# Performance work log

Measured on AMD Instinct MI355X. Metric: run time of the kernel, lower is better.

Reference implementation:

```python
import jax, jax.numpy as jnp
import numpy as np

N, E, F, H = 50000, 800000, 256, 64


def setup_inputs() -> dict:
    key = jax.random.key(0)
    ks = jax.random.split(key, 6)
    x = jax.random.normal(ks[0], (N, F), jnp.float32)
    edge_index = jax.random.randint(ks[1], (2, E), 0, N)
    init = lambda k, shp, fan: jax.random.normal(k, shp, jnp.float32) / np.float32(np.sqrt(fan))
    W1l = init(ks[2], (F, H), F)
    b1l = jnp.zeros((H,), jnp.float32)
    W1r = init(ks[3], (F, H), F)
    W2l = init(ks[4], (H, H), H)
    b2l = jnp.zeros((H,), jnp.float32)
    W2r = init(ks[5], (H, H), H)
    return dict(x=x, edge_index=edge_index, W1l=W1l, b1l=b1l, W1r=W1r,
                W2l=W2l, b2l=b2l, W2r=W2r)


def _sage(x, src, dst, Wl, bl, Wr, n):
    # SAGEConv: out = mean_{j->i}(lin_l(x)_j) + lin_r(x)_i
    m = x @ Wl + bl                                   # [N, H]
    agg = jax.ops.segment_sum(m[src], dst, num_segments=n)
    deg = jax.ops.segment_sum(jnp.ones((src.shape[0],), x.dtype), dst, num_segments=n)
    agg = agg / jnp.maximum(deg, 1.0)[:, None]        # mean aggregation
    return agg + x @ Wr


def reference(x, edge_index, W1l, b1l, W1r, W2l, b2l, W2r):
    src, dst = edge_index[0], edge_index[1]
    n = x.shape[0]
    # 2-layer SAGE encoder (dropout=0, no residual for 2 layers)
    h = jax.nn.relu(_sage(x, src, dst, W1l, b1l, W1r, n))
    z = _sage(h, src, dst, W2l, b2l, W2r, n)
    # UnitNorm: replace all-zero rows with randn, then row-wise L2 normalize
    valid = jnp.sum(z != 0, axis=1, keepdims=True) > 0
    r = jax.random.normal(jax.random.key(42), z.shape, z.dtype)
    z = jnp.where(valid, z, r)
    z = z / jnp.sqrt(jnp.sum(z * z, axis=1, keepdims=True))
    # dot-product decode on observed edges + positive-edge BCE loss
    scores = jnp.sum(z[src] * z[dst], axis=-1)        # [E]
    loss = -jnp.mean(jax.nn.log_sigmoid(scores))
    return z, loss
```

## Files before the change

kernel.cpp:

```cpp
#include <hip/hip_runtime.h>

#define N_NODES 50000
#define N_EDGES 800000
#define F_IN    256
#define H_DIM   64
#define NB_SCAN ((N_NODES + 255) / 256)
#define TILE_A  4096
#define EPT     (TILE_A / 256)
#define MAXB    5632
#define GT1     ((N_NODES + 63) / 64)
#define SUBN    64
#define DEC_GRID ((N_NODES + SUBN - 1) / SUBN)

typedef __attribute__((ext_vector_type(8))) short short8;
typedef __attribute__((ext_vector_type(4))) float floatx4;

__device__ __forceinline__ unsigned short f2bf(float f) {
  unsigned int u;
  __builtin_memcpy(&u, &f, 4);
  u += 0x7fffu + ((u >> 16) & 1u);
  return (unsigned short)(u >> 16);
}
__device__ __forceinline__ float bf2f(unsigned short s) {
  unsigned int v = ((unsigned int)s) << 16; float f; __builtin_memcpy(&f, &v, 4); return f;
}
__device__ __forceinline__ float bflo(unsigned int u) {
  unsigned int v = u << 16; float f; __builtin_memcpy(&f, &v, 4); return f;
}
__device__ __forceinline__ float bfhi(unsigned int u) {
  unsigned int v = u & 0xffff0000u; float f; __builtin_memcpy(&f, &v, 4); return f;
}

template<int K>
__device__ __forceinline__ void pack_body(int t, const float* __restrict__ Wl,
                                          const float* __restrict__ Wr,
                                          unsigned short* __restrict__ Wb)
{
  int lane = t & 63;
  int f    = t >> 6;
  int m    = f & 1;
  int c    = (f >> 1) & 3;
  int ks   = f >> 3;
  const float* W = m ? Wr : Wl;
  int quad = lane >> 4, l15 = lane & 15;
  int col = c * 16 + l15;
  unsigned short u[8];
#pragma unroll
  for (int j = 0; j < 8; ++j) {
    int k = ks * 32 + quad * 8 + j;
    u[j] = f2bf(W[k * H_DIM + col]);
  }
  uint4 v;
  __builtin_memcpy(&v, u, 16);
  ((uint4*)Wb)[t] = v;
}

__global__ __launch_bounds__(256) void pack_all_k(
    const float* __restrict__ W1l, const float* __restrict__ W1r,
    const float* __restrict__ W2l, const float* __restrict__ W2r,
    unsigned short* __restrict__ Wb1, unsigned short* __restrict__ Wb2,
    float* __restrict__ loss_slot, int* __restrict__ bcur)
{
  if (blockIdx.x == 0) {
    if (threadIdx.x == 0) loss_slot[0] = 0.f;
    if (threadIdx.x < NB_SCAN) bcur[threadIdx.x] = 0;
  }
  int b = blockIdx.x;
  if (b < 16) {
    pack_body<F_IN>(b * 256 + threadIdx.x, W1l, W1r, Wb1);
  } else {
    pack_body<H_DIM>((b - 16) * 256 + threadIdx.x, W2l, W2r, Wb2);
  }
}

template<int K, bool XBF16>
__device__ __forceinline__ void gemm_body(
    int bx, unsigned short* xs,
    const void* __restrict__ X_,
    const unsigned short* __restrict__ Wb,
    const float* __restrict__ bl,
    unsigned short* __restrict__ outl, unsigned short* __restrict__ outr)
{
  constexpr int KP = K + 8;
  const int row0 = bx * 64;
  if (XBF16) {
    const uint4* X = (const uint4*)X_;
    const int CH = K / 8;
    for (int i = threadIdx.x; i < 64 * CH; i += 256) {
      int r = i / CH, c = i % CH;
      int row = row0 + r;
      uint4 v = (row < N_NODES) ? X[(size_t)row * CH + c] : make_uint4(0, 0, 0, 0);
      *(uint4*)&xs[r * KP + c * 8] = v;
    }
  } else {
    const float4* X = (const float4*)X_;
    const int CH = K / 4;
    for (int i = threadIdx.x; i < 64 * CH; i += 256) {
      int r = i / CH, c = i % CH;
      int row = row0 + r;
      float4 v = (row < N_NODES) ? X[(size_t)row * CH + c]
                                 : make_float4(0.f, 0.f, 0.f, 0.f);
      unsigned int lo = (unsigned int)f2bf(v.x) | ((unsigned int)f2bf(v.y) << 16);
      unsigned int hi = (unsigned int)f2bf(v.z) | ((unsigned int)f2bf(v.w) << 16);
      *(uint2*)&xs[r * KP + c * 4] = make_uint2(lo, hi);
    }
// ... 10 lines not shown
#pragma unroll
  for (int c = 0; c < 4; ++c) { accl[c] = (floatx4)0.f; accr[c] = (floatx4)0.f; }

  const uint4* wbase = (const uint4*)Wb;
#pragma unroll
  for (int ks = 0; ks < K / 32; ++ks) {
    short8 af = *(const short8*)&xs[rloc * KP + ks * 32 + quad * 8];
#pragma unroll
    for (int c = 0; c < 4; ++c) {
      uint4 rl = wbase[((ks * 4 + c) * 2 + 0) * 64 + lane];
      uint4 rr = wbase[((ks * 4 + c) * 2 + 1) * 64 + lane];
      short8 bfl, bfr;
      __builtin_memcpy(&bfl, &rl, 16);
      __builtin_memcpy(&bfr, &rr, 16);
      accl[c] = __builtin_amdgcn_mfma_f32_16x16x32_bf16(af, bfl, accl[c], 0, 0, 0);
      accr[c] = __builtin_amdgcn_mfma_f32_16x16x32_bf16(af, bfr, accr[c], 0, 0, 0);
    }
  }
#pragma unroll
  for (int c = 0; c < 4; ++c) {
    int col = c * 16 + l15;
    float bias = bl[col];
#pragma unroll
    for (int reg = 0; reg < 4; ++reg) {
      int row = row0 + w * 16 + quad * 4 + reg;
      if (row < N_NODES) {
        outl[(size_t)row * H_DIM + col] = f2bf(accl[c][reg] + bias);
        outr[(size_t)row * H_DIM + col] = f2bf(accr[c][reg]);
      }
    }
  }
}

__global__ __launch_bounds__(256) void binA_k(const int* __restrict__ ei,
                                              int* __restrict__ bcur,
                                              unsigned int* __restrict__ ebuf)
{
  __shared__ int lcnt[256];
  __shared__ int lofs[256];
  __shared__ int lstart[256];
  __shared__ int gstart[256];
  __shared__ int lcur[256];
  __shared__ unsigned int ldata[TILE_A];
  const int t = threadIdx.x;
  const int e0 = blockIdx.x * TILE_A;
  lcnt[t] = 0;
  __syncthreads();
  int ss[EPT], ds[EPT];
#pragma unroll
  for (int j = 0; j < EPT; ++j) {
    int e = e0 + t + j * 256;
    if (e < N_EDGES) {
      ss[j] = ei[e];
      ds[j] = ei[N_EDGES + e];
      atomicAdd(&lcnt[ds[j] >> 8], 1);
    } else {
      ds[j] = -1;
    }
  }
  __syncthreads();
  int v = lcnt[t];
  lofs[t] = v;
  __syncthreads();
  for (int off = 1; off < 256; off <<= 1) {
    int u = (t >= off) ? lofs[t - off] : 0;
    __syncthreads();
    lofs[t] += u;
    __syncthreads();
  }
  lstart[t] = lofs[t] - v;
  lcur[t]   = lofs[t] - v;
  if (t < NB_SCAN && v > 0) gstart[t] = atomicAdd(&bcur[t], v);
  __syncthreads();
#pragma unroll
  for (int j = 0; j < EPT; ++j) {
    if (ds[j] >= 0) {
      int p = atomicAdd(&lcur[ds[j] >> 8], 1);
      ldata[p] = ((unsigned int)ss[j] << 8) | (unsigned int)(ds[j] & 255);
// ... 38 lines not shown
  __syncthreads();
  const int start = sh_se[0], len = sh_se[1];
  const unsigned int* eb = ebuf + (size_t)b * MAXB;
  ncnt[t] = 0;
  __syncthreads();
  for (int i = t; i < len; i += 256) atomicAdd(&ncnt[eb[i] & 255], 1);
  __syncthreads();
  int v = ncnt[t];
  nscan[t] = v;
  __syncthreads();
  for (int off = 1; off < 256; off <<= 1) {
    int u = (t >= off) ? nscan[t - off] : 0;
    __syncthreads();
    nscan[t] += u;
    __syncthreads();
  }
  ncur[t] = nscan[t] - v;
  __syncthreads();
  for (int i = t; i < len; i += 256) {
    unsigned int e = eb[i];
    int p = atomicAdd(&ncur[e & 255], 1);
    sdata[p] = e >> 8;
  }
  __syncthreads();
  for (int i = t; i < len; i += 256) esrc[start + i] = (int)sdata[i];
  int node = b * 256 + t;
  int s0 = start + nscan[t] - v;
  if (node < N_NODES) {
    rowptr[node] = s0;
    if (node == N_NODES - 1) rowptr[N_NODES] = s0 + v;
  }
}

__global__ __launch_bounds__(256, 4) void binB_gemm1_k(
    const float* __restrict__ x, const unsigned short* __restrict__ Wb1,
    const float* __restrict__ b1l,
    unsigned short* __restrict__ m1, unsigned short* __restrict__ xr,
    const unsigned int* __restrict__ ebuf, const int* __restrict__ bcur,
    int* __restrict__ esrc, int* __restrict__ rowptr)
{
  __shared__ __align__(16) unsigned char smem[64 * (F_IN + 8) * 2];
  if (blockIdx.x < GT1) {
    gemm_body<F_IN, false>(blockIdx.x, (unsigned short*)smem, x, Wb1, b1l, m1, xr);
  } else {
    binB_body(blockIdx.x - GT1, smem, ebuf, bcur, esrc, rowptr);
  }
}

__global__ __launch_bounds__(256, 4) void gemm2_k(
    const void* __restrict__ X_, const unsigned short* __restrict__ Wb,
    const float* __restrict__ bl,
    unsigned short* __restrict__ outl, unsigned short* __restrict__ outr)
{
  __shared__ __align__(16) unsigned short xs[64 * (H_DIM + 8)];
  gemm_body<H_DIM, true>(blockIdx.x, xs, X_, Wb, bl, outl, outr);
}

__device__ __forceinline__ void agg_quad(const int* __restrict__ esrc,
                                         const unsigned short* __restrict__ m,
                                         int b, int e, int g, int l15,
                                         float* __restrict__ a)
{
  float a0 = 0.f, a1 = 0.f, a2 = 0.f, a3 = 0.f;
  float b0 = 0.f, b1 = 0.f, b2 = 0.f, b3 = 0.f;
  int i = b + g;
  for (; i + 4 < e; i += 8) {
    int s0 = esrc[i], s1 = esrc[i + 4];
    uint2 v0 = *(const uint2*)(m + (size_t)s0 * H_DIM + l15 * 4);
    uint2 v1 = *(const uint2*)(m + (size_t)s1 * H_DIM + l15 * 4);
    a0 += bflo(v0.x); a1 += bfhi(v0.x); a2 += bflo(v0.y); a3 += bfhi(v0.y);
    b0 += bflo(v1.x); b1 += bfhi(v1.x); b2 += bflo(v1.y); b3 += bfhi(v1.y);
  }
  if (i < e) {
    int s0 = esrc[i];
    uint2 v0 = *(const uint2*)(m + (size_t)s0 * H_DIM + l15 * 4);
    a0 += bflo(v0.x); a1 += bfhi(v0.x); a2 += bflo(v0.y); a3 += bfhi(v0.y);
  }
  a[0] = a0 + b0; a[1] = a1 + b1; a[2] = a2 + b2; a[3] = a3 + b3;
#pragma unroll
  for (int j = 0; j < 4; ++j) {
    a[j] += __shfl_xor(a[j], 16, 64);
    a[j] += __shfl_xor(a[j], 32, 64);
  }
}

__global__ __launch_bounds__(256) void agg1_k(
    const int* __restrict__ rowptr, const int* __restrict__ esrc,
    const unsigned short* __restrict__ m, const unsigned short* __restrict__ xr,
    unsigned short* __restrict__ h)
{
  int gid = blockIdx.x * 256 + threadIdx.x;
  int row = gid >> 6;
  if (row >= N_NODES) return;
  int lane = threadIdx.x & 63, g = lane >> 4, l15 = lane & 15;
  int b = rowptr[row], e = rowptr[row + 1];
  float a[4];
  agg_quad(esrc, m, b, e, g, l15, a);
  if (g == 0) {
    float dv = fmaxf((float)(e - b), 1.f);
    float inv = 1.f / dv;
    uint2 rx = *(const uint2*)(xr + (size_t)row * H_DIM + l15 * 4);
    float h0 = fmaxf(a[0] * inv + bflo(rx.x), 0.f);
    float h1 = fmaxf(a[1] * inv + bfhi(rx.x), 0.f);
    float h2 = fmaxf(a[2] * inv + bflo(rx.y), 0.f);
    float h3 = fmaxf(a[3] * inv + bfhi(rx.y), 0.f);
    uint2 o;
    o.x = (unsigned int)f2bf(h0) | ((unsigned int)f2bf(h1) << 16);
    o.y = (unsigned int)f2bf(h2) | ((unsigned int)f2bf(h3) << 16);
    *(uint2*)(h + (size_t)row * H_DIM + l15 * 4) = o;
  }
}

__global__ __launch_bounds__(256) void agg2_k(
    const int* __restrict__ rowptr, const int* __restrict__ esrc,
    const unsigned short* __restrict__ m, const unsigned short* __restrict__ hr,
    float* __restrict__ zout, unsigned short* __restrict__ zb)
{
  int gid = blockIdx.x * 256 + threadIdx.x;
  int row = gid >> 6;
  if (row >= N_NODES) return;
  int lane = threadIdx.x & 63, g = lane >> 4, l15 = lane & 15;
  int b = rowptr[row], e = rowptr[row + 1];
  float a[4];
  agg_quad(esrc, m, b, e, g, l15, a);
  float dv = fmaxf((float)(e - b), 1.f);
  float inv = 1.f / dv;
  uint2 rx = *(const uint2*)(hr + (size_t)row * H_DIM + l15 * 4);
  float v0 = a[0] * inv + bflo(rx.x);
  float v1 = a[1] * inv + bfhi(rx.x);
  float v2 = a[2] * inv + bflo(rx.y);
  float v3 = a[3] * inv + bfhi(rx.y);
  float ss = v0 * v0 + v1 * v1 + v2 * v2 + v3 * v3;
#pragma unroll
  for (int mm = 8; mm >= 1; mm >>= 1) ss += __shfl_xor(ss, mm, 64);
  float rs = rsqrtf(fmaxf(ss, 1e-30f));
  if (g == 0) {
    float z0 = v0 * rs, z1 = v1 * rs, z2 = v2 * rs, z3 = v3 * rs;
    *(float4*)(zout + (size_t)row * H_DIM + l15 * 4) = make_float4(z0, z1, z2, z3);
    uint2 o;
    o.x = (unsigned int)f2bf(z0) | ((unsigned int)f2bf(z1) << 16);
    o.y = (unsigned int)f2bf(z2) | ((unsigned int)f2bf(z3) << 16);
    *(uint2*)(zb + (size_t)row * H_DIM + l15 * 4) = o;
  }
}

__global__ __launch_bounds__(256) void decode_lds_k(
    const int* __restrict__ rowptr, const int* __restrict__ esrc,
    const unsigned short* __restrict__ zb, float* __restrict__ loss_slot)
{
  __shared__ __align__(16) uint4 zrows[SUBN * 8];
  __shared__ int sh_rp[SUBN + 1];
  const int t = threadIdx.x;
  const int node0 = blockIdx.x * SUBN;
  const int nr = min(SUBN, N_NODES - node0);
  for (int i = t; i < nr * 8; i += 256) {
    int r = i >> 3, c = i & 7;
    uint4 v = ((const uint4*)(zb + (size_t)(node0 + r) * H_DIM))[c];
    zrows[r * 8 + (c ^ (r & 7))] = v;
  }
  if (t <= nr) sh_rp[t] = rowptr[node0 + t];
  __syncthreads();
  const int estart = sh_rp[0], eend = sh_rp[nr];
  float part = 0.f;
  for (int e = estart + t; e < eend; e += 512) {
    int e2 = e + 256;
    bool has2 = (e2 < eend);
    int lo = 0, hi = nr;
    while (hi - lo > 1) {
      int mid = (lo + hi) >> 1;
      if (sh_rp[mid] <= e) lo = mid; else hi = mid;
    }
    const int r1 = lo;
    hi = nr;
    while (hi - lo > 1) {
      int mid = (lo + hi) >> 1;
      if (sh_rp[mid] <= e2) lo = mid; else hi = mid;
    }
    const int r2 = lo;
    const int s1 = esrc[e];
    const int s2 = has2 ? esrc[e2] : s1;
    const uint4* zs1 = (const uint4*)(zb + (size_t)s1 * H_DIM);
    const uint4* zs2 = (const uint4*)(zb + (size_t)s2 * H_DIM);
    float p1 = 0.f, p2 = 0.f;
#pragma unroll
    for (int c = 0; c < 8; ++c) {
      uint4 a1 = zs1[c], b1 = zrows[r1 * 8 + (c ^ (r1 & 7))];
      uint4 a2 = zs2[c], b2 = zrows[r2 * 8 + (c ^ (r2 & 7))];
      unsigned int au1[4] = {a1.x, a1.y, a1.z, a1.w};
      unsigned int bu1[4] = {b1.x, b1.y, b1.z, b1.w};
      unsigned int au2[4] = {a2.x, a2.y, a2.z, a2.w};
      unsigned int bu2[4] = {b2.x, b2.y, b2.z, b2.w};
#pragma unroll
      for (int j = 0; j < 4; ++j) {
        p1 = fmaf(bflo(au1[j]), bflo(bu1[j]), p1);
        p1 = fmaf(bfhi(au1[j]), bfhi(bu1[j]), p1);
        p2 = fmaf(bflo(au2[j]), bflo(bu2[j]), p2);
        p2 = fmaf(bfhi(au2[j]), bfhi(bu2[j]), p2);
      }
    }
    part += fmaxf(-p1, 0.f) + log1pf(expf(-fabsf(p1)));
    if (has2) part += fmaxf(-p2, 0.f) + log1pf(expf(-fabsf(p2)));
  }
#pragma unroll
  for (int m = 32; m >= 1; m >>= 1) part += __shfl_xor(part, m, 64);
  __shared__ float sbuf[4];
  int lane = t & 63, w = t >> 6;
  if (lane == 0) sbuf[w] = part;
  __syncthreads();
  if (t == 0)
    atomicAdd(loss_slot, (sbuf[0] + sbuf[1] + sbuf[2] + sbuf[3]) * (1.0f / N_EDGES));
}

extern "C" void kernel_launch(void* const* d_in, const int* in_sizes, int n_in,
                              void* d_out, int out_size, void* d_ws, size_t ws_size,
                              hipStream_t stream)
{
  (void)in_sizes; (void)n_in; (void)out_size; (void)ws_size;
  const float* x   = (const float*)d_in[0];
  const int*   ei  = (const int*)d_in[1];
  const float* W1l = (const float*)d_in[2];
  const float* b1l = (const float*)d_in[3];
  const float* W1r = (const float*)d_in[4];
  const float* W2l = (const float*)d_in[5];
  const float* b2l = (const float*)d_in[6];
  const float* W2r = (const float*)d_in[7];
  float* out = (float*)d_out;
  float* loss_slot = out + (size_t)N_NODES * H_DIM;

  const size_t NH = (size_t)N_NODES * H_DIM;
  unsigned short* uA = (unsigned short*)d_ws;
  unsigned short* uB = uA + NH;
  unsigned short* uC = uB + NH;
  unsigned short* Wb1 = uC + NH;
  unsigned short* Wb2 = Wb1 + (F_IN / 32) * 4 * 2 * 64 * 8;
  int* rowptr = (int*)(Wb2 + (H_DIM / 32) * 4 * 2 * 64 * 8);
  int* esrc   = rowptr + N_NODES + 1;
  int* bcur   = esrc + N_EDGES;
  unsigned int* ebuf = (unsigned int*)(bcur + NB_SCAN);

  dim3 blk(256);
  dim3 g_node((N_NODES * 64 + 255) / 256);
  dim3 g_binA((N_EDGES + TILE_A - 1) / TILE_A);
  dim3 g_fuse(GT1 + NB_SCAN);
  dim3 g_tile(GT1);
  dim3 g_dec(DEC_GRID);

  pack_all_k<<<dim3(20), blk, 0, stream>>>(W1l, W1r, W2l, W2r, Wb1, Wb2,
                                           loss_slot, bcur);
  binA_k<<<g_binA, blk, 0, stream>>>(ei, bcur, ebuf);
  binB_gemm1_k<<<g_fuse, blk, 0, stream>>>(x, Wb1, b1l, uA, uC,
                                           ebuf, bcur, esrc, rowptr);
  agg1_k<<<g_node, blk, 0, stream>>>(rowptr, esrc, uA, uC, uB);
  gemm2_k<<<g_tile, blk, 0, stream>>>(uB, Wb2, b2l, uA, uC);
  agg2_k<<<g_node, blk, 0, stream>>>(rowptr, esrc, uA, uC, out, uB);
  decode_lds_k<<<g_dec, blk, 0, stream>>>(rowptr, esrc, uB, loss_slot);
}
```

Before: 236.7 us.

## Fuse all stages into one cooperative persistent kernel with grid syncs

Replaces the seven separate kernel launches with a single cooperative persistent kernel that loops over work items for each stage and separates the stages with grid-wide barriers. It also halves the binA edge tile. The aim is to remove per-launch overhead and the gaps between dependent kernels. The trade-offs are lower occupancy, because the grid is capped by co-resident blocks and the kernel needs registers for every stage, plus grid-sync cost and load imbalance inside each phase. The old multi-kernel path is kept as a fallback.

Result: slower. 715.1 us (+202.1%).

```diff
diff --git a/kernel.cpp b/kernel.cpp
--- a/kernel.cpp
+++ b/kernel.cpp
@@ -1,16 +1,22 @@
 #include <hip/hip_runtime.h>
+#include <hip/hip_cooperative_groups.h>
+
+namespace cg = cooperative_groups;
 
 #define N_NODES 50000
 #define N_EDGES 800000
 #define F_IN    256
 #define H_DIM   64
 #define NB_SCAN ((N_NODES + 255) / 256)
-#define TILE_A  4096
+#define TILE_A  2048
 #define EPT     (TILE_A / 256)
+#define NT_A    ((N_EDGES + TILE_A - 1) / TILE_A)
 #define MAXB    5632
 #define GT1     ((N_NODES + 63) / 64)
 #define SUBN    64
 #define DEC_GRID ((N_NODES + SUBN - 1) / SUBN)
+#define AGG_VB  ((N_NODES + 3) / 4)
+#define SMEM_BYTES (64 * (F_IN + 8) * 2)
 
 typedef __attribute__((ext_vector_type(8))) short short8;
 typedef __attribute__((ext_vector_type(4))) float floatx4;
@@ -30,6 +36,7 @@
 __device__ __forceinline__ float bfhi(unsigned int u) {
   unsigned int v = u & 0xffff0000u; float f; __builtin_memcpy(&f, &v, 4); return f;
 }
+
 
 template<int K>
 __device__ __forceinline__ void pack_body(int t, const float* __restrict__ Wl,
@@ -53,24 +60,6 @@
   uint4 v;
   __builtin_memcpy(&v, u, 16);
   ((uint4*)Wb)[t] = v;
-}
-
-__global__ __launch_bounds__(256) void pack_all_k(
-    const float* __restrict__ W1l, const float* __restrict__ W1r,
-    const float* __restrict__ W2l, const float* __restrict__ W2r,
-    unsigned short* __restrict__ Wb1, unsigned short* __restrict__ Wb2,
-    float* __restrict__ loss_slot, int* __restrict__ bcur)
-{
-  if (blockIdx.x == 0) {
-    if (threadIdx.x == 0) loss_slot[0] = 0.f;
-    if (threadIdx.x < NB_SCAN) bcur[threadIdx.x] = 0;
-  }
-  int b = blockIdx.x;
-  if (b < 16) {
-    pack_body<F_IN>(b * 256 + threadIdx.x, W1l, W1r, Wb1);
-  } else {
-    pack_body<H_DIM>((b - 16) * 256 + threadIdx.x, W2l, W2r, Wb2);
-  }
 }
 
 template<int K, bool XBF16>
@@ -147,18 +136,19 @@
   }
 }
 
-__global__ __launch_bounds__(256) void binA_k(const int* __restrict__ ei,
-                                              int* __restrict__ bcur,
-                                              unsigned int* __restrict__ ebuf)
-{
-  __shared__ int lcnt[256];
-  __shared__ int lofs[256];
-  __shared__ int lstart[256];
-  __shared__ int gstart[256];
-  __shared__ int lcur[256];
-  __shared__ unsigned int ldata[TILE_A];
+__device__ __forceinline__ void binA_body(int blk, unsigned char* smem,
+                                          const int* __restrict__ ei,
+                                          int* __restrict__ bcur,
+                                          unsigned int* __restrict__ ebuf)
+{
+  int* lcnt   = (int*)smem;
+  int* lofs   = lcnt + 256;
+  int* lstart = lofs + 256;
+  int* gstart = lstart + 256;
+  int* lcur   = gstart + 256;
+  unsigned int* ldata = (unsigned int*)(lcur + 256);
   const int t = threadIdx.x;
-  const int e0 = blockIdx.x * TILE_A;
+  const int e0 = blk * TILE_A;
   lcnt[t] = 0;
   __syncthreads();
   int ss[EPT], ds[EPT];
@@ -263,30 +253,6 @@
   }
 }
 
-__global__ __launch_bounds__(256, 4) void binB_gemm1_k(
-    const float* __restrict__ x, const unsigned short* __restrict__ Wb1,
-    const float* __restrict__ b1l,
-    unsigned short* __restrict__ m1, unsigned short* __restrict__ xr,
-    const unsigned int* __restrict__ ebuf, const int* __restrict__ bcur,
-    int* __restrict__ esrc, int* __restrict__ rowptr)
-{
-  __shared__ __align__(16) unsigned char smem[64 * (F_IN + 8) * 2];
-  if (blockIdx.x < GT1) {
-    gemm_body<F_IN, false>(blockIdx.x, (unsigned short*)smem, x, Wb1, b1l, m1, xr);
-  } else {
-    binB_body(blockIdx.x - GT1, smem, ebuf, bcur, esrc, rowptr);
-  }
-}
-
-__global__ __launch_bounds__(256, 4) void gemm2_k(
-    const void* __restrict__ X_, const unsigned short* __restrict__ Wb,
-    const float* __restrict__ bl,
-    unsigned short* __restrict__ outl, unsigned short* __restrict__ outr)
-{
-  __shared__ __align__(16) unsigned short xs[64 * (H_DIM + 8)];
-  gemm_body<H_DIM, true>(blockIdx.x, xs, X_, Wb, bl, outl, outr);
-}
-
 __device__ __forceinline__ void agg_quad(const int* __restrict__ esrc,
                                          const unsigned short* __restrict__ m,
                                          int b, int e, int g, int l15,
@@ -315,21 +281,16 @@
   }
 }
 
-__global__ __launch_bounds__(256) void agg1_k(
+__device__ __forceinline__ void agg1_row(int row,
     const int* __restrict__ rowptr, const int* __restrict__ esrc,
     const unsigned short* __restrict__ m, const unsigned short* __restrict__ xr,
-    unsigned short* __restrict__ h)
-{
-  int gid = blockIdx.x * 256 + threadIdx.x;
-  int row = gid >> 6;
-  if (row >= N_NODES) return;
-  int lane = threadIdx.x & 63, g = lane >> 4, l15 = lane & 15;
+    unsigned short* __restrict__ h, int g, int l15)
+{
   int b = rowptr[row], e = rowptr[row + 1];
   float a[4];
   agg_quad(esrc, m, b, e, g, l15, a);
   if (g == 0) {
-    float dv = fmaxf((float)(e - b), 1.f);
-    float inv = 1.f / dv;
+    float inv = 1.f / fmaxf((float)(e - b), 1.f);
     uint2 rx = *(const uint2*)(xr + (size_t)row * H_DIM + l15 * 4);
     float h0 = fmaxf(a[0] * inv + bflo(rx.x), 0.f);
     float h1 = fmaxf(a[1] * inv + bfhi(rx.x), 0.f);
@@ -342,20 +303,15 @@
   }
 }
 
-__global__ __launch_bounds__(256) void agg2_k(
+__device__ __forceinline__ void agg2_row(int row,
     const int* __restrict__ rowptr, const int* __restrict__ esrc,
     const unsigned short* __restrict__ m, const unsigned short* __restrict__ hr,
-    float* __restrict__ zout, unsigned short* __restrict__ zb)
-{
-  int gid = blockIdx.x * 256 + threadIdx.x;
-  int row = gid >> 6;
-  if (row >= N_NODES) return;
-  int lane = threadIdx.x & 63, g = lane >> 4, l15 = lane & 15;
+    float* __restrict__ zout, unsigned short* __restrict__ zb, int g, int l15)
+{
   int b = rowptr[row], e = rowptr[row + 1];
   float a[4];
   agg_quad(esrc, m, b, e, g, l15, a);
-  float dv = fmaxf((float)(e - b), 1.f);
-  float inv = 1.f / dv;
+  float inv = 1.f / fmaxf((float)(e - b), 1.f);
   uint2 rx = *(const uint2*)(hr + (size_t)row * H_DIM + l15 * 4);
   float v0 = a[0] * inv + bflo(rx.x);
   float v1 = a[1] * inv + bfhi(rx.x);
@@ -375,14 +331,15 @@
   }
 }
 
-__global__ __launch_bounds__(256) void decode_lds_k(
+__device__ __forceinline__ void decode_body(int wb, unsigned char* smem,
     const int* __restrict__ rowptr, const int* __restrict__ esrc,
     const unsigned short* __restrict__ zb, float* __restrict__ loss_slot)
 {
-  __shared__ __align__(16) uint4 zrows[SUBN * 8];
-  __shared__ int sh_rp[SUBN + 1];
+  uint4* zrows = (uint4*)smem;
+  int*   sh_rp = (int*)(smem + 8192);
+  float* sbuf  = (float*)(smem + 8192 + 272);
   const int t = threadIdx.x;
-  const int node0 = blockIdx.x * SUBN;
+  const int node0 = wb * SUBN;
   const int nr = min(SUBN, N_NODES - node0);
   for (int i = t; i < nr * 8; i += 256) {
     int r = i >> 3, c = i & 7;
@@ -434,12 +391,151 @@
   }
 #pragma unroll
   for (int m = 32; m >= 1; m >>= 1) part += __shfl_xor(part, m, 64);
-  __shared__ float sbuf[4];
   int lane = t & 63, w = t >> 6;
   if (lane == 0) sbuf[w] = part;
   __syncthreads();
   if (t == 0)
     atomicAdd(loss_slot, (sbuf[0] + sbuf[1] + sbuf[2] + sbuf[3]) * (1.0f / N_EDGES));
+}
+
+__global__ __launch_bounds__(256, 4) void mega_k(
+    const float* __restrict__ x, const int* __restrict__ ei,
+    const float* __restrict__ W1l, const float* __restrict__ b1l,
+    const float* __restrict__ W1r, const float* __restrict__ W2l,
+    const float* __restrict__ b2l, const float* __restrict__ W2r,
+    float* __restrict__ out, float* __restrict__ loss_slot,
+    unsigned short* __restrict__ uA, unsigned short* __restrict__ uB,
+    unsigned short* __restrict__ uC, unsigned short* __restrict__ Wb1,
+    unsigned short* __restrict__ Wb2, int* __restrict__ rowptr,
+    int* __restrict__ esrc, int* __restrict__ bcur,
+    unsigned int* __restrict__ ebuf)
+{
+  __shared__ __align__(16) unsigned char smem[SMEM_BYTES];
+  cg::grid_group gg = cg::this_grid();
+  const int t = threadIdx.x;
+  const int lane = t & 63, qg = lane >> 4, l15 = lane & 15, wv = t >> 6;
+
+  if (blockIdx.x < 16) {
+    pack_body<F_IN>(blockIdx.x * 256 + t, W1l, W1r, Wb1);
+  } else if (blockIdx.x < 20) {
+    pack_body<H_DIM>((blockIdx.x - 16) * 256 + t, W2l, W2r, Wb2);
+  } else if (blockIdx.x == 20) {
+    if (t == 0) loss_slot[0] = 0.f;
+    if (t < NB_SCAN) bcur[t] = 0;
+  }
+  gg.sync();
+
+  for (int blk = blockIdx.x; blk < NT_A; blk += gridDim.x) {
+    binA_body(blk, smem, ei, bcur, ebuf);
+    __syncthreads();
+  }
+  gg.sync();
+
+  for (int w = blockIdx.x; w < GT1 + NB_SCAN; w += gridDim.x) {
+    if (w < GT1) gemm_body<F_IN, false>(w, (unsigned short*)smem, x, Wb1, b1l, uA, uC);
+    else         binB_body(w - GT1, smem, ebuf, bcur, esrc, rowptr);
+    __syncthreads();
+  }
+  gg.sync();
+
+  for (int vb = blockIdx.x; vb < AGG_VB; vb += gridDim.x) {
+    int row = vb * 4 + wv;
+    if (row < N_NODES) agg1_row(row, rowptr, esrc, uA, uC, uB, qg, l15);
+  }
+  gg.sync();
+
+  for (int bx = blockIdx.x; bx < GT1; bx += gridDim.x) {
+    gemm_body<H_DIM, true>(bx, (unsigned short*)smem, uB, Wb2, b2l, uA, uC);
+    __syncthreads();
+  }
+  gg.sync();
+
+  for (int vb = blockIdx.x; vb < AGG_VB; vb += gridDim.x) {
+    int row = vb * 4 + wv;
+    if (row < N_NODES) agg2_row(row, rowptr, esrc, uA, uC, out, uB, qg, l15);
+  }
+  gg.sync();
+
+  for (int w = blockIdx.x; w < DEC_GRID; w += gridDim.x) {
+    decode_body(w, smem, rowptr, esrc, uB, loss_slot);
+    __syncthreads();
+  }
+}
+
+__global__ __launch_bounds__(256) void pack_all_k(
+    const float* __restrict__ W1l, const float* __restrict__ W1r,
+    const float* __restrict__ W2l, const float* __restrict__ W2r,
+    unsigned short* __restrict__ Wb1, unsigned short* __restrict__ Wb2,
+    float* __restrict__ loss_slot, int* __restrict__ bcur)
+{
+  if (blockIdx.x == 0) {
+    if (threadIdx.x == 0) loss_slot[0] = 0.f;
+    if (threadIdx.x < NB_SCAN) bcur[threadIdx.x] = 0;
+  }
+  int b = blockIdx.x;
+  if (b < 16) pack_body<F_IN>(b * 256 + threadIdx.x, W1l, W1r, Wb1);
+  else        pack_body<H_DIM>((b - 16) * 256 + threadIdx.x, W2l, W2r, Wb2);
+}
+
+__global__ __launch_bounds__(256) void binA_k(const int* __restrict__ ei,
+                                              int* __restrict__ bcur,
+                                              unsigned int* __restrict__ ebuf)
+{
+  __shared__ __align__(16) unsigned char smem[5 * 1024 + TILE_A * 4];
+  binA_body(blockIdx.x, smem, ei, bcur, ebuf);
+}
+
+__global__ __launch_bounds__(256, 4) void binB_gemm1_k(
+    const float* __restrict__ x, const unsigned short* __restrict__ Wb1,
+    const float* __restrict__ b1l,
+    unsigned short* __restrict__ m1, unsigned short* __restrict__ xr,
+    const unsigned int* __restrict__ ebuf, const int* __restrict__ bcur,
+    int* __restrict__ esrc, int* __restrict__ rowptr)
+{
+  __shared__ __align__(16) unsigned char smem[SMEM_BYTES];
+  if (blockIdx.x < GT1) gemm_body<F_IN, false>(blockIdx.x, (unsigned short*)smem, x, Wb1, b1l, m1, xr);
+  else                  binB_body(blockIdx.x - GT1, smem, ebuf, bcur, esrc, rowptr);
+}
+
+__global__ __launch_bounds__(256, 4) void gemm2_k(
+    const void* __restrict__ X_, const unsigned short* __restrict__ Wb,
+    const float* __restrict__ bl,
+    unsigned short* __restrict__ outl, unsigned short* __restrict__ outr)
+{
+  __shared__ __align__(16) unsigned short xs[64 * (H_DIM + 8)];
+  gemm_body<H_DIM, true>(blockIdx.x, xs, X_, Wb, bl, outl, outr);
+}
+
+__global__ __launch_bounds__(256) void agg1_k(
+    const int* __restrict__ rowptr, const int* __restrict__ esrc,
+    const unsigned short* __restrict__ m, const unsigned short* __restrict__ xr,
+    unsigned short* __restrict__ h)
+{
+  int gid = blockIdx.x * 256 + threadIdx.x;
+  int row = gid >> 6;
+  if (row >= N_NODES) return;
+  int lane = threadIdx.x & 63;
+  agg1_row(row, rowptr, esrc, m, xr, h, lane >> 4, lane & 15);
+}
+
+__global__ __launch_bounds__(256) void agg2_k(
+    const int* __restrict__ rowptr, const int* __restrict__ esrc,
+    const unsigned short* __restrict__ m, const unsigned short* __restrict__ hr,
+    float* __restrict__ zout, unsigned short* __restrict__ zb)
+{
+  int gid = blockIdx.x * 256 + threadIdx.x;
+  int row = gid >> 6;
+  if (row >= N_NODES) return;
+  int lane = threadIdx.x & 63;
+  agg2_row(row, rowptr, esrc, m, hr, zout, zb, lane >> 4, lane & 15);
+}
+
+__global__ __launch_bounds__(256) void decode_lds_k(
+    const int* __restrict__ rowptr, const int* __restrict__ esrc,
+    const unsigned short* __restrict__ zb, float* __restrict__ loss_slot)
+{
+  __shared__ __align__(16) unsigned char smem[8480];
+  decode_body(blockIdx.x, smem, rowptr, esrc, zb, loss_slot);
 }
 
 extern "C" void kernel_launch(void* const* d_in, const int* in_sizes, int n_in,
@@ -469,20 +565,41 @@
   int* bcur   = esrc + N_EDGES;
   unsigned int* ebuf = (unsigned int*)(bcur + NB_SCAN);
 
-  dim3 blk(256);
-  dim3 g_node((N_NODES * 64 + 255) / 256);
-  dim3 g_binA((N_EDGES + TILE_A - 1) / TILE_A);
-  dim3 g_fuse(GT1 + NB_SCAN);
-  dim3 g_tile(GT1);
-  dim3 g_dec(DEC_GRID);
-
-  pack_all_k<<<dim3(20), blk, 0, stream>>>(W1l, W1r, W2l, W2r, Wb1, Wb2,
-                                           loss_slot, bcur);
-  binA_k<<<g_binA, blk, 0, stream>>>(ei, bcur, ebuf);
-  binB_gemm1_k<<<g_fuse, blk, 0, stream>>>(x, Wb1, b1l, uA, uC,
-                                           ebuf, bcur, esrc, rowptr);
-  agg1_k<<<g_node, blk, 0, stream>>>(rowptr, esrc, uA, uC, uB);
-  gemm2_k<<<g_tile, blk, 0, stream>>>(uB, Wb2, b2l, uA, uC);
-  agg2_k<<<g_node, blk, 0, stream>>>(rowptr, esrc, uA, uC, out, uB);
-  decode_lds_k<<<g_dec, blk, 0, stream>>>(rowptr, esrc, uB, loss_slot);
-}
+  static int g_grid = 0;
+  if (g_grid == 0) {
+    int nb = 0;
+    hipError_t e = hipOccupancyMaxActiveBlocksPerMultiprocessor(&nb, mega_k, 256, 0);
+    int dev = 0;
+    hipGetDevice(&dev);
+    hipDeviceProp_t prop;
+    hipGetDeviceProperties(&prop, dev);
+    long cap = (e == hipSuccess && nb > 0) ? (long)nb * prop.multiProcessorCount : 0;
+    g_grid = (cap <= 0) ? -1 : (int)(cap < 1024 ? cap : 1024);
+  }
+
+  bool coop_ok = false;
+  if (g_grid > 0) {
+    void* params[] = {
+      (void*)&x, (void*)&ei, (void*)&W1l, (void*)&b1l, (void*)&W1r,
+      (void*)&W2l, (void*)&b2l, (void*)&W2r, (void*)&out, (void*)&loss_slot,
+      (void*)&uA, (void*)&uB, (void*)&uC, (void*)&Wb1, (void*)&Wb2,
+      (void*)&rowptr, (void*)&esrc, (void*)&bcur, (void*)&ebuf};
+    hipError_t e = hipLaunchCooperativeKernel((const void*)mega_k, dim3(g_grid),
+                                              dim3(256), params, 0, stream);
+    coop_ok = (e == hipSuccess);
+    if (!coop_ok) g_grid = -1;
+  }
+
+  if (!coop_ok) {
+    dim3 blk(256);
+    pack_all_k<<<dim3(20), blk, 0, stream>>>(W1l, W1r, W2l, W2r, Wb1, Wb2,
+                                             loss_slot, bcur);
+    binA_k<<<dim3(NT_A), blk, 0, stream>>>(ei, bcur, ebuf);
+    binB_gemm1_k<<<dim3(GT1 + NB_SCAN), blk, 0, stream>>>(x, Wb1, b1l, uA, uC,
+                                                          ebuf, bcur, esrc, rowptr);
+    agg1_k<<<dim3((N_NODES * 64 + 255) / 256), blk, 0, stream>>>(rowptr, esrc, uA, uC, uB);
+    gemm2_k<<<dim3(GT1), blk, 0, stream>>>(uB, Wb2, b2l, uA, uC);
+    agg2_k<<<dim3((N_NODES * 64 + 255) / 256), blk, 0, stream>>>(rowptr, esrc, uA, uC, out, uB);
+    decode_lds_k<<<dim3(DEC_GRID), blk, 0, stream>>>(rowptr, esrc, uB, loss_slot);
+  }
+}
```

## Fuse layer-1 aggregation with layer-2 GEMM and unroll gather loop deeper

Applied to the files above, without the earlier changes.

Merges the first-layer mean aggregation and the second-layer dual linear projection into one kernel. Each 512-thread block aggregates 64 rows into shared memory as bf16 h, then four waves run MFMA against the packed W2 weights, so h is never written to or re-read from global memory and one launch goes away. New buffers uD/uE are used to avoid read/write aliasing with the layer-1 outputs. The gather loop in agg_quad now keeps four independent accumulator sets and issues four loads per iteration for more memory-level parallelism. The cost is fewer blocks (one per 64 rows) with half the waves idle during the GEMM phase, and more register pressure in the gather loop.

New measurement: 255.9 us. 1.08x slower.

```diff
diff --git a/kernel.cpp b/kernel.cpp
--- a/kernel.cpp
+++ b/kernel.cpp
@@ -66,11 +66,8 @@
     if (threadIdx.x < NB_SCAN) bcur[threadIdx.x] = 0;
   }
   int b = blockIdx.x;
-  if (b < 16) {
-    pack_body<F_IN>(b * 256 + threadIdx.x, W1l, W1r, Wb1);
-  } else {
-    pack_body<H_DIM>((b - 16) * 256 + threadIdx.x, W2l, W2r, Wb2);
-  }
+  if (b < 16) pack_body<F_IN>(b * 256 + threadIdx.x, W1l, W1r, Wb1);
+  else        pack_body<H_DIM>((b - 16) * 256 + threadIdx.x, W2l, W2r, Wb2);
 }
 
 template<int K, bool XBF16>
@@ -271,20 +268,8 @@
     int* __restrict__ esrc, int* __restrict__ rowptr)
 {
   __shared__ __align__(16) unsigned char smem[64 * (F_IN + 8) * 2];
-  if (blockIdx.x < GT1) {
-    gemm_body<F_IN, false>(blockIdx.x, (unsigned short*)smem, x, Wb1, b1l, m1, xr);
-  } else {
-    binB_body(blockIdx.x - GT1, smem, ebuf, bcur, esrc, rowptr);
-  }
-}
-
-__global__ __launch_bounds__(256, 4) void gemm2_k(
-    const void* __restrict__ X_, const unsigned short* __restrict__ Wb,
-    const float* __restrict__ bl,
-    unsigned short* __restrict__ outl, unsigned short* __restrict__ outr)
-{
-  __shared__ __align__(16) unsigned short xs[64 * (H_DIM + 8)];
-  gemm_body<H_DIM, true>(blockIdx.x, xs, X_, Wb, bl, outl, outr);
+  if (blockIdx.x < GT1) gemm_body<F_IN, false>(blockIdx.x, (unsigned short*)smem, x, Wb1, b1l, m1, xr);
+  else                  binB_body(blockIdx.x - GT1, smem, ebuf, bcur, esrc, rowptr);
 }
 
 __device__ __forceinline__ void agg_quad(const int* __restrict__ esrc,
@@ -292,22 +277,31 @@
                                          int b, int e, int g, int l15,
                                          float* __restrict__ a)
 {
-  float a0 = 0.f, a1 = 0.f, a2 = 0.f, a3 = 0.f;
-  float b0 = 0.f, b1 = 0.f, b2 = 0.f, b3 = 0.f;
+  float p0 = 0.f, p1 = 0.f, p2 = 0.f, p3 = 0.f;
+  float q0 = 0.f, q1 = 0.f, q2 = 0.f, q3 = 0.f;
+  float r0 = 0.f, r1 = 0.f, r2 = 0.f, r3 = 0.f;
+  float s0 = 0.f, s1 = 0.f, s2 = 0.f, s3 = 0.f;
   int i = b + g;
-  for (; i + 4 < e; i += 8) {
-    int s0 = esrc[i], s1 = esrc[i + 4];
-    uint2 v0 = *(const uint2*)(m + (size_t)s0 * H_DIM + l15 * 4);
-    uint2 v1 = *(const uint2*)(m + (size_t)s1 * H_DIM + l15 * 4);
-    a0 += bflo(v0.x); a1 += bfhi(v0.x); a2 += bflo(v0.y); a3 += bfhi(v0.y);
-    b0 += bflo(v1.x); b1 += bfhi(v1.x); b2 += bflo(v1.y); b3 += bfhi(v1.y);
-  }
-  if (i < e) {
-    int s0 = esrc[i];
-    uint2 v0 = *(const uint2*)(m + (size_t)s0 * H_DIM + l15 * 4);
-    a0 += bflo(v0.x); a1 += bfhi(v0.x); a2 += bflo(v0.y); a3 += bfhi(v0.y);
-  }
-  a[0] = a0 + b0; a[1] = a1 + b1; a[2] = a2 + b2; a[3] = a3 + b3;
+  for (; i + 12 < e; i += 16) {
+    int sa = esrc[i], sb = esrc[i + 4], sc = esrc[i + 8], sd = esrc[i + 12];
+    uint2 va = *(const uint2*)(m + (size_t)sa * H_DIM + l15 * 4);
+    uint2 vb = *(const uint2*)(m + (size_t)sb * H_DIM + l15 * 4);
+    uint2 vc = *(const uint2*)(m + (size_t)sc * H_DIM + l15 * 4);
+    uint2 vd = *(const uint2*)(m + (size_t)sd * H_DIM + l15 * 4);
+    p0 += bflo(va.x); p1 += bfhi(va.x); p2 += bflo(va.y); p3 += bfhi(va.y);
+    q0 += bflo(vb.x); q1 += bfhi(vb.x); q2 += bflo(vb.y); q3 += bfhi(vb.y);
+    r0 += bflo(vc.x); r1 += bfhi(vc.x); r2 += bflo(vc.y); r3 += bfhi(vc.y);
+    s0 += bflo(vd.x); s1 += bfhi(vd.x); s2 += bflo(vd.y); s3 += bfhi(vd.y);
+  }
+  for (; i < e; i += 4) {
+    int sa = esrc[i];
+    uint2 va = *(const uint2*)(m + (size_t)sa * H_DIM + l15 * 4);
+    p0 += bflo(va.x); p1 += bfhi(va.x); p2 += bflo(va.y); p3 += bfhi(va.y);
+  }
+  a[0] = (p0 + q0) + (r0 + s0);
+  a[1] = (p1 + q1) + (r1 + s1);
+  a[2] = (p2 + q2) + (r2 + s2);
+  a[3] = (p3 + q3) + (r3 + s3);
 #pragma unroll
   for (int j = 0; j < 4; ++j) {
     a[j] += __shfl_xor(a[j], 16, 64);
@@ -315,10 +309,86 @@
   }
 }
 
-__global__ __launch_bounds__(256) void agg1_k(
+__global__ __launch_bounds__(512) void agg1gemm2_k(
     const int* __restrict__ rowptr, const int* __restrict__ esrc,
-    const unsigned short* __restrict__ m, const unsigned short* __restrict__ xr,
-    unsigned short* __restrict__ h)
+    const unsigned short* __restrict__ m1, const unsigned short* __restrict__ xr,
+    const unsigned short* __restrict__ Wb, const float* __restrict__ bl,
+    unsigned short* __restrict__ outl, unsigned short* __restrict__ outr)
+{
+  constexpr int KP = H_DIM + 8;
+  __shared__ __align__(16) unsigned short xs[64 * KP];
+  const int t = threadIdx.x;
+  const int wv = t >> 6;
+  const int lane = t & 63;
+  const int g = lane >> 4, l15 = lane & 15;
+  const int row0 = blockIdx.x * 64;
+
+  for (int k = 0; k < 8; ++k) {
+    int r = wv * 8 + k;
+    int row = row0 + r;
+    if (row < N_NODES) {
+      int b = rowptr[row], e = rowptr[row + 1];
+      float a[4];
+      agg_quad(esrc, m1, b, e, g, l15, a);
+      if (g == 0) {
+        float inv = 1.f / fmaxf((float)(e - b), 1.f);
+        uint2 rx = *(const uint2*)(xr + (size_t)row * H_DIM + l15 * 4);
+        float h0 = fmaxf(a[0] * inv + bflo(rx.x), 0.f);
+        float h1 = fmaxf(a[1] * inv + bfhi(rx.x), 0.f);
+        float h2 = fmaxf(a[2] * inv + bflo(rx.y), 0.f);
+        float h3 = fmaxf(a[3] * inv + bfhi(rx.y), 0.f);
+        uint2 o;
+        o.x = (unsigned int)f2bf(h0) | ((unsigned int)f2bf(h1) << 16);
+        o.y = (unsigned int)f2bf(h2) | ((unsigned int)f2bf(h3) << 16);
+        *(uint2*)&xs[r * KP + l15 * 4] = o;
+      }
+    } else if (g == 0) {
+      *(uint2*)&xs[r * KP + l15 * 4] = make_uint2(0u, 0u);
+    }
+  }
+  __syncthreads();
+
+  if (wv < 4) {
+    const int quad = lane >> 4;
+    const int rloc = wv * 16 + l15;
+    floatx4 accl[4], accr[4];
+#pragma unroll
+    for (int c = 0; c < 4; ++c) { accl[c] = (floatx4)0.f; accr[c] = (floatx4)0.f; }
+    const uint4* wbase = (const uint4*)Wb;
+#pragma unroll
+    for (int ks = 0; ks < 2; ++ks) {
+      short8 af = *(const short8*)&xs[rloc * KP + ks * 32 + quad * 8];
+#pragma unroll
+      for (int c = 0; c < 4; ++c) {
+        uint4 rl = wbase[((ks * 4 + c) * 2 + 0) * 64 + lane];
+        uint4 rr = wbase[((ks * 4 + c) * 2 + 1) * 64 + lane];
+        short8 bfl, bfr;
+        __builtin_memcpy(&bfl, &rl, 16);
+        __builtin_memcpy(&bfr, &rr, 16);
+        accl[c] = __builtin_amdgcn_mfma_f32_16x16x32_bf16(af, bfl, accl[c], 0, 0, 0);
+        accr[c] = __builtin_amdgcn_mfma_f32_16x16x32_bf16(af, bfr, accr[c], 0, 0, 0);
+      }
+    }
+#pragma unroll
+    for (int c = 0; c < 4; ++c) {
+      int col = c * 16 + l15;
+      float bias = bl[col];
+#pragma unroll
+      for (int reg = 0; reg < 4; ++reg) {
+        int row = row0 + wv * 16 + quad * 4 + reg;
+        if (row < N_NODES) {
+          outl[(size_t)row * H_DIM + col] = f2bf(accl[c][reg] + bias);
+          outr[(size_t)row * H_DIM + col] = f2bf(accr[c][reg]);
+        }
+      }
+    }
+  }
+}
+
+__global__ __launch_bounds__(256) void agg2_k(
+    const int* __restrict__ rowptr, const int* __restrict__ esrc,
+    const unsigned short* __restrict__ m, const unsigned short* __restrict__ hr,
+    float* __restrict__ zout, unsigned short* __restrict__ zb)
 {
   int gid = blockIdx.x * 256 + threadIdx.x;
   int row = gid >> 6;
@@ -327,35 +397,7 @@
   int b = rowptr[row], e = rowptr[row + 1];
   float a[4];
   agg_quad(esrc, m, b, e, g, l15, a);
-  if (g == 0) {
-    float dv = fmaxf((float)(e - b), 1.f);
-    float inv = 1.f / dv;
-    uint2 rx = *(const uint2*)(xr + (size_t)row * H_DIM + l15 * 4);
-    float h0 = fmaxf(a[0] * inv + bflo(rx.x), 0.f);
-    float h1 = fmaxf(a[1] * inv + bfhi(rx.x), 0.f);
-    float h2 = fmaxf(a[2] * inv + bflo(rx.y), 0.f);
-    float h3 = fmaxf(a[3] * inv + bfhi(rx.y), 0.f);
-    uint2 o;
-    o.x = (unsigned int)f2bf(h0) | ((unsigned int)f2bf(h1) << 16);
-    o.y = (unsigned int)f2bf(h2) | ((unsigned int)f2bf(h3) << 16);
-    *(uint2*)(h + (size_t)row * H_DIM + l15 * 4) = o;
-  }
-}
-
-__global__ __launch_bounds__(256) void agg2_k(
-    const int* __restrict__ rowptr, const int* __restrict__ esrc,
-    const unsigned short* __restrict__ m, const unsigned short* __restrict__ hr,
-    float* __restrict__ zout, unsigned short* __restrict__ zb)
-{
-  int gid = blockIdx.x * 256 + threadIdx.x;
-  int row = gid >> 6;
-  if (row >= N_NODES) return;
-  int lane = threadIdx.x & 63, g = lane >> 4, l15 = lane & 15;
-  int b = rowptr[row], e = rowptr[row + 1];
-  float a[4];
-  agg_quad(esrc, m, b, e, g, l15, a);
-  float dv = fmaxf((float)(e - b), 1.f);
-  float inv = 1.f / dv;
+  float inv = 1.f / fmaxf((float)(e - b), 1.f);
   uint2 rx = *(const uint2*)(hr + (size_t)row * H_DIM + l15 * 4);
   float v0 = a[0] * inv + bflo(rx.x);
   float v1 = a[1] * inv + bfhi(rx.x);
@@ -462,7 +504,9 @@
   unsigned short* uA = (unsigned short*)d_ws;
   unsigned short* uB = uA + NH;
   unsigned short* uC = uB + NH;
-  unsigned short* Wb1 = uC + NH;
+  unsigned short* uD = uC + NH;
+  unsigned short* uE = uD + NH;
+  unsigned short* Wb1 = uE + NH;
   unsigned short* Wb2 = Wb1 + (F_IN / 32) * 4 * 2 * 64 * 8;
   int* rowptr = (int*)(Wb2 + (H_DIM / 32) * 4 * 2 * 64 * 8);
   int* esrc   = rowptr + N_NODES + 1;
@@ -470,10 +514,10 @@
   unsigned int* ebuf = (unsigned int*)(bcur + NB_SCAN);
 
   dim3 blk(256);
-  dim3 g_node((N_NODES * 64 + 255) / 256);
   dim3 g_binA((N_EDGES + TILE_A - 1) / TILE_A);
   dim3 g_fuse(GT1 + NB_SCAN);
   dim3 g_tile(GT1);
+  dim3 g_node((N_NODES * 64 + 255) / 256);
   dim3 g_dec(DEC_GRID);
 
   pack_all_k<<<dim3(20), blk, 0, stream>>>(W1l, W1r, W2l, W2r, Wb1, Wb2,
@@ -481,8 +525,8 @@
   binA_k<<<g_binA, blk, 0, stream>>>(ei, bcur, ebuf);
   binB_gemm1_k<<<g_fuse, blk, 0, stream>>>(x, Wb1, b1l, uA, uC,
                                            ebuf, bcur, esrc, rowptr);
-  agg1_k<<<g_node, blk, 0, stream>>>(rowptr, esrc, uA, uC, uB);
-  gemm2_k<<<g_tile, blk, 0, stream>>>(uB, Wb2, b2l, uA, uC);
-  agg2_k<<<g_node, blk, 0, stream>>>(rowptr, esrc, uA, uC, out, uB);
+  agg1gemm2_k<<<g_tile, dim3(512), 0, stream>>>(rowptr, esrc, uA, uC,
+                                                Wb2, b2l, uD, uE);
+  agg2_k<<<g_node, blk, 0, stream>>>(rowptr, esrc, uD, uE, out, uB);
   decode_lds_k<<<g_dec, blk, 0, stream>>>(rowptr, esrc, uB, loss_slot);
 }
```

## Store normalized embeddings as FP8 for decode and unroll aggregation gathers deeper

Applied to the files above, without the earlier changes.

agg2 now writes the normalized z rows as packed FP8 (e4m3-style via cvt_pk_fp8) instead of bf16, and the decode kernel reads these 64-byte rows and converts them back with hardware pack conversions before the dot products. This halves the gather traffic in the edge-wise decode loss. Separately, the neighbor aggregation loop is unrolled to four independent gathers per iteration to raise memory-level parallelism. The FP8 path lowers the precision of the edge scores and so of the loss, which may hurt tolerance.

Result: no change. 233.2 us (-1.5%).

```diff
diff --git a/kernel.cpp b/kernel.cpp
--- a/kernel.cpp
+++ b/kernel.cpp
@@ -14,6 +14,7 @@
 
 typedef __attribute__((ext_vector_type(8))) short short8;
 typedef __attribute__((ext_vector_type(4))) float floatx4;
+typedef __attribute__((ext_vector_type(2))) float floatx2;
 
 __device__ __forceinline__ unsigned short f2bf(float f) {
   unsigned int u;
@@ -29,6 +30,18 @@
 }
 __device__ __forceinline__ float bfhi(unsigned int u) {
   unsigned int v = u & 0xffff0000u; float f; __builtin_memcpy(&f, &v, 4); return f;
+}
+
+__device__ __forceinline__ float dot4_fp8(unsigned int a, unsigned int b, float acc) {
+  floatx2 a01 = __builtin_amdgcn_cvt_pk_f32_fp8(a, false);
+  floatx2 a23 = __builtin_amdgcn_cvt_pk_f32_fp8(a, true);
+  floatx2 b01 = __builtin_amdgcn_cvt_pk_f32_fp8(b, false);
+  floatx2 b23 = __builtin_amdgcn_cvt_pk_f32_fp8(b, true);
+  acc = fmaf(a01[0], b01[0], acc);
+  acc = fmaf(a01[1], b01[1], acc);
+  acc = fmaf(a23[0], b23[0], acc);
+  acc = fmaf(a23[1], b23[1], acc);
+  return acc;
 }
 
 template<int K>
@@ -66,11 +79,8 @@
     if (threadIdx.x < NB_SCAN) bcur[threadIdx.x] = 0;
   }
   int b = blockIdx.x;
-  if (b < 16) {
-    pack_body<F_IN>(b * 256 + threadIdx.x, W1l, W1r, Wb1);
-  } else {
-    pack_body<H_DIM>((b - 16) * 256 + threadIdx.x, W2l, W2r, Wb2);
-  }
+  if (b < 16) pack_body<F_IN>(b * 256 + threadIdx.x, W1l, W1r, Wb1);
+  else        pack_body<H_DIM>((b - 16) * 256 + threadIdx.x, W2l, W2r, Wb2);
 }
 
 template<int K, bool XBF16>
@@ -271,11 +281,8 @@
     int* __restrict__ esrc, int* __restrict__ rowptr)
 {
   __shared__ __align__(16) unsigned char smem[64 * (F_IN + 8) * 2];
-  if (blockIdx.x < GT1) {
-    gemm_body<F_IN, false>(blockIdx.x, (unsigned short*)smem, x, Wb1, b1l, m1, xr);
-  } else {
-    binB_body(blockIdx.x - GT1, smem, ebuf, bcur, esrc, rowptr);
-  }
+  if (blockIdx.x < GT1) gemm_body<F_IN, false>(blockIdx.x, (unsigned short*)smem, x, Wb1, b1l, m1, xr);
+  else                  binB_body(blockIdx.x - GT1, smem, ebuf, bcur, esrc, rowptr);
 }
 
 __global__ __launch_bounds__(256, 4) void gemm2_k(
@@ -292,22 +299,31 @@
                                          int b, int e, int g, int l15,
                                          float* __restrict__ a)
 {
-  float a0 = 0.f, a1 = 0.f, a2 = 0.f, a3 = 0.f;
-  float b0 = 0.f, b1 = 0.f, b2 = 0.f, b3 = 0.f;
+  float p0 = 0.f, p1 = 0.f, p2 = 0.f, p3 = 0.f;
+  float q0 = 0.f, q1 = 0.f, q2 = 0.f, q3 = 0.f;
+  float r0 = 0.f, r1 = 0.f, r2 = 0.f, r3 = 0.f;
+  float s0 = 0.f, s1 = 0.f, s2 = 0.f, s3 = 0.f;
   int i = b + g;
-  for (; i + 4 < e; i += 8) {
-    int s0 = esrc[i], s1 = esrc[i + 4];
-    uint2 v0 = *(const uint2*)(m + (size_t)s0 * H_DIM + l15 * 4);
-    uint2 v1 = *(const uint2*)(m + (size_t)s1 * H_DIM + l15 * 4);
-    a0 += bflo(v0.x); a1 += bfhi(v0.x); a2 += bflo(v0.y); a3 += bfhi(v0.y);
-    b0 += bflo(v1.x); b1 += bfhi(v1.x); b2 += bflo(v1.y); b3 += bfhi(v1.y);
-  }
-  if (i < e) {
-    int s0 = esrc[i];
-    uint2 v0 = *(const uint2*)(m + (size_t)s0 * H_DIM + l15 * 4);
-    a0 += bflo(v0.x); a1 += bfhi(v0.x); a2 += bflo(v0.y); a3 += bfhi(v0.y);
-  }
-  a[0] = a0 + b0; a[1] = a1 + b1; a[2] = a2 + b2; a[3] = a3 + b3;
+  for (; i + 12 < e; i += 16) {
+    int sa = esrc[i], sb = esrc[i + 4], sc = esrc[i + 8], sd = esrc[i + 12];
+    uint2 va = *(const uint2*)(m + (size_t)sa * H_DIM + l15 * 4);
+    uint2 vb = *(const uint2*)(m + (size_t)sb * H_DIM + l15 * 4);
+    uint2 vc = *(const uint2*)(m + (size_t)sc * H_DIM + l15 * 4);
+    uint2 vd = *(const uint2*)(m + (size_t)sd * H_DIM + l15 * 4);
+    p0 += bflo(va.x); p1 += bfhi(va.x); p2 += bflo(va.y); p3 += bfhi(va.y);
+    q0 += bflo(vb.x); q1 += bfhi(vb.x); q2 += bflo(vb.y); q3 += bfhi(vb.y);
+    r0 += bflo(vc.x); r1 += bfhi(vc.x); r2 += bflo(vc.y); r3 += bfhi(vc.y);
+    s0 += bflo(vd.x); s1 += bfhi(vd.x); s2 += bflo(vd.y); s3 += bfhi(vd.y);
+  }
+  for (; i < e; i += 4) {
+    int sa = esrc[i];
+    uint2 va = *(const uint2*)(m + (size_t)sa * H_DIM + l15 * 4);
+    p0 += bflo(va.x); p1 += bfhi(va.x); p2 += bflo(va.y); p3 += bfhi(va.y);
+  }
+  a[0] = (p0 + q0) + (r0 + s0);
+  a[1] = (p1 + q1) + (r1 + s1);
+  a[2] = (p2 + q2) + (r2 + s2);
+  a[3] = (p3 + q3) + (r3 + s3);
 #pragma unroll
   for (int j = 0; j < 4; ++j) {
     a[j] += __shfl_xor(a[j], 16, 64);
@@ -328,8 +344,7 @@
   float a[4];
   agg_quad(esrc, m, b, e, g, l15, a);
   if (g == 0) {
-    float dv = fmaxf((float)(e - b), 1.f);
-    float inv = 1.f / dv;
+    float inv = 1.f / fmaxf((float)(e - b), 1.f);
     uint2 rx = *(const uint2*)(xr + (size_t)row * H_DIM + l15 * 4);
     float h0 = fmaxf(a[0] * inv + bflo(rx.x), 0.f);
     float h1 = fmaxf(a[1] * inv + bfhi(rx.x), 0.f);
@@ -345,7 +360,7 @@
 __global__ __launch_bounds__(256) void agg2_k(
     const int* __restrict__ rowptr, const int* __restrict__ esrc,
     const unsigned short* __restrict__ m, const unsigned short* __restrict__ hr,
-    float* __restrict__ zout, unsigned short* __restrict__ zb)
+    float* __restrict__ zout, unsigned char* __restrict__ zb8)
 {
   int gid = blockIdx.x * 256 + threadIdx.x;
   int row = gid >> 6;
@@ -354,8 +369,7 @@
   int b = rowptr[row], e = rowptr[row + 1];
   float a[4];
   agg_quad(esrc, m, b, e, g, l15, a);
-  float dv = fmaxf((float)(e - b), 1.f);
-  float inv = 1.f / dv;
+  float inv = 1.f / fmaxf((float)(e - b), 1.f);
   uint2 rx = *(const uint2*)(hr + (size_t)row * H_DIM + l15 * 4);
   float v0 = a[0] * inv + bflo(rx.x);
   float v1 = a[1] * inv + bfhi(rx.x);
@@ -368,26 +382,26 @@
   if (g == 0) {
     float z0 = v0 * rs, z1 = v1 * rs, z2 = v2 * rs, z3 = v3 * rs;
     *(float4*)(zout + (size_t)row * H_DIM + l15 * 4) = make_float4(z0, z1, z2, z3);
-    uint2 o;
-    o.x = (unsigned int)f2bf(z0) | ((unsigned int)f2bf(z1) << 16);
-    o.y = (unsigned int)f2bf(z2) | ((unsigned int)f2bf(z3) << 16);
-    *(uint2*)(zb + (size_t)row * H_DIM + l15 * 4) = o;
-  }
-}
-
-__global__ __launch_bounds__(256) void decode_lds_k(
+    unsigned int w8 = (unsigned int)__builtin_amdgcn_cvt_pk_fp8_f32(z0, z1, 0, false);
+    w8 = (unsigned int)__builtin_amdgcn_cvt_pk_fp8_f32(z2, z3, (int)w8, true);
+    ((unsigned int*)(zb8 + (size_t)row * H_DIM))[l15] = w8;
+  }
+}
+
+__global__ __launch_bounds__(256) void decode_fp8_k(
     const int* __restrict__ rowptr, const int* __restrict__ esrc,
-    const unsigned short* __restrict__ zb, float* __restrict__ loss_slot)
-{
-  __shared__ __align__(16) uint4 zrows[SUBN * 8];
+    const unsigned char* __restrict__ zb8, float* __restrict__ loss_slot)
+{
+  __shared__ __align__(16) unsigned int zrows[SUBN * 16];
   __shared__ int sh_rp[SUBN + 1];
+  __shared__ float sbuf[4];
   const int t = threadIdx.x;
   const int node0 = blockIdx.x * SUBN;
   const int nr = min(SUBN, N_NODES - node0);
-  for (int i = t; i < nr * 8; i += 256) {
-    int r = i >> 3, c = i & 7;
-    uint4 v = ((const uint4*)(zb + (size_t)(node0 + r) * H_DIM))[c];
-    zrows[r * 8 + (c ^ (r & 7))] = v;
+  for (int i = t; i < nr * 16; i += 256) {
+    int r = i >> 4, c = i & 15;
+    unsigned int w = ((const unsigned int*)(zb8 + (size_t)(node0 + r) * H_DIM))[c];
+    zrows[r * 16 + (c ^ (r & 15))] = w;
   }
   if (t <= nr) sh_rp[t] = rowptr[node0 + t];
   __syncthreads();
@@ -410,23 +424,21 @@
     const int r2 = lo;
     const int s1 = esrc[e];
     const int s2 = has2 ? esrc[e2] : s1;
-    const uint4* zs1 = (const uint4*)(zb + (size_t)s1 * H_DIM);
-    const uint4* zs2 = (const uint4*)(zb + (size_t)s2 * H_DIM);
+    const uint4* zs1 = (const uint4*)(zb8 + (size_t)s1 * H_DIM);
+    const uint4* zs2 = (const uint4*)(zb8 + (size_t)s2 * H_DIM);
     float p1 = 0.f, p2 = 0.f;
 #pragma unroll
-    for (int c = 0; c < 8; ++c) {
-      uint4 a1 = zs1[c], b1 = zrows[r1 * 8 + (c ^ (r1 & 7))];
-      uint4 a2 = zs2[c], b2 = zrows[r2 * 8 + (c ^ (r2 & 7))];
+    for (int c4 = 0; c4 < 4; ++c4) {
+      uint4 a1 = zs1[c4], a2 = zs2[c4];
       unsigned int au1[4] = {a1.x, a1.y, a1.z, a1.w};
-      unsigned int bu1[4] = {b1.x, b1.y, b1.z, b1.w};
       unsigned int au2[4] = {a2.x, a2.y, a2.z, a2.w};
-      unsigned int bu2[4] = {b2.x, b2.y, b2.z, b2.w};
 #pragma unroll
       for (int j = 0; j < 4; ++j) {
-        p1 = fmaf(bflo(au1[j]), bflo(bu1[j]), p1);
-        p1 = fmaf(bfhi(au1[j]), bfhi(bu1[j]), p1);
-        p2 = fmaf(bflo(au2[j]), bflo(bu2[j]), p2);
-        p2 = fmaf(bfhi(au2[j]), bfhi(bu2[j]), p2);
+        int c = c4 * 4 + j;
+        unsigned int b1 = zrows[r1 * 16 + (c ^ (r1 & 15))];
+        unsigned int b2 = zrows[r2 * 16 + (c ^ (r2 & 15))];
+        p1 = dot4_fp8(au1[j], b1, p1);
+        p2 = dot4_fp8(au2[j], b2, p2);
       }
     }
     part += fmaxf(-p1, 0.f) + log1pf(expf(-fabsf(p1)));
@@ -434,7 +446,6 @@
   }
 #pragma unroll
   for (int m = 32; m >= 1; m >>= 1) part += __shfl_xor(part, m, 64);
-  __shared__ float sbuf[4];
   int lane = t & 63, w = t >> 6;
   if (lane == 0) sbuf[w] = part;
   __syncthreads();
@@ -462,6 +473,7 @@
   unsigned short* uA = (unsigned short*)d_ws;
   unsigned short* uB = uA + NH;
   unsigned short* uC = uB + NH;
+  unsigned char*  zb8 = (unsigned char*)uB;
   unsigned short* Wb1 = uC + NH;
   unsigned short* Wb2 = Wb1 + (F_IN / 32) * 4 * 2 * 64 * 8;
   int* rowptr = (int*)(Wb2 + (H_DIM / 32) * 4 * 2 * 64 * 8);
@@ -470,10 +482,10 @@
   unsigned int* ebuf = (unsigned int*)(bcur + NB_SCAN);
 
   dim3 blk(256);
-  dim3 g_node((N_NODES * 64 + 255) / 256);
   dim3 g_binA((N_EDGES + TILE_A - 1) / TILE_A);
   dim3 g_fuse(GT1 + NB_SCAN);
   dim3 g_tile(GT1);
+  dim3 g_node((N_NODES * 64 + 255) / 256);
   dim3 g_dec(DEC_GRID);
 
   pack_all_k<<<dim3(20), blk, 0, stream>>>(W1l, W1r, W2l, W2r, Wb1, Wb2,
@@ -483,6 +495,6 @@
                                            ebuf, bcur, esrc, rowptr);
   agg1_k<<<g_node, blk, 0, stream>>>(rowptr, esrc, uA, uC, uB);
   gemm2_k<<<g_tile, blk, 0, stream>>>(uB, Wb2, b2l, uA, uC);
-  agg2_k<<<g_node, blk, 0, stream>>>(rowptr, esrc, uA, uC, out, uB);
-  decode_lds_k<<<g_dec, blk, 0, stream>>>(rowptr, esrc, uB, loss_slot);
-}
+  agg2_k<<<g_node, blk, 0, stream>>>(rowptr, esrc, uA, uC, out, zb8);
+  decode_fp8_k<<<g_dec, blk, 0, stream>>>(rowptr, esrc, zb8, loss_slot);
+}
```
